# Optimization experiments

Hardware: AMD Instinct MI355X
Metric: run time of the kernel (lower is better)

## Reference

```python
import jax, jax.numpy as jnp
import numpy as np

B, T, D = 1, 2048, 3072
N, K, H = 16, 8, 256  # heads, kv heads, head dim
SOFT_CAP = 50.0
WINDOW = 1024
ROPE_BASE = 10000.0
ROPE_SCALE = 1.0
K_MASK = -2.3819763e+38
EPS = 1e-6


def rms_norm(x, scale=None):
    var = jnp.mean(jnp.square(x), axis=-1, keepdims=True)
    y = x * jax.lax.rsqrt(var + EPS)
    if scale is not None:
        y = y * (1.0 + scale)
    return y


def apply_rope(x, positions):
    # x: [B, T, n, H], positions: [B, T] int
    half = x.shape[-1] // 2
    fraction = 2.0 * jnp.arange(half, dtype=jnp.float32) / x.shape[-1]
    timescale = ROPE_BASE ** fraction  # [half]
    sinusoid = positions[..., None].astype(jnp.float32) / timescale  # [B,T,half]
    sinusoid = sinusoid[..., None, :] / ROPE_SCALE  # [B,T,1,half]
    sin, cos = jnp.sin(sinusoid), jnp.cos(sinusoid)
    first, second = jnp.split(x, 2, axis=-1)
    out = jnp.concatenate([first * cos - second * sin,
                           second * cos + first * sin], axis=-1)
    return out.astype(x.dtype)


def setup_inputs() -> dict:
    key = jax.random.key(0)
    ks = jax.random.split(key, 6)
    x = jax.random.normal(ks[0], (B, T, D), jnp.float32)
    segment_pos = jnp.broadcast_to(jnp.arange(T, dtype=jnp.int32), (B, T))
    attn_mask = jnp.broadcast_to(jnp.tril(jnp.ones((T, T), bool)), (B, T, T))
    w_q = jax.random.normal(ks[1], (N, D, H), jnp.float32) * 0.02
    w_kv = jax.random.normal(ks[2], (2, K, D, H), jnp.float32) * 0.02
    w_out = jax.random.normal(ks[3], (N, H, D), jnp.float32) * 0.02
    q_scale = jax.random.normal(ks[4], (H,), jnp.float32) * 0.1
    k_scale = jax.random.normal(ks[5], (H,), jnp.float32) * 0.1
    return {"x": x, "segment_pos": segment_pos, "attn_mask": attn_mask,
            "w_q": w_q, "w_kv": w_kv, "w_out": w_out,
            "q_scale": q_scale, "k_scale": k_scale}


def reference(x, segment_pos, attn_mask, w_q, w_kv, w_out, q_scale, k_scale):
    # Q projection + QK-RMSNorm + RoPE
    q = jnp.einsum('BTD,NDH->BTNH', x, w_q)
    q = rms_norm(q, q_scale)
    q = apply_rope(q, segment_pos)
    # fused KV projection
    kv = jnp.einsum('BSD,CKDH->CBSKH', x, w_kv)
    k_proj, v_proj = kv[0], kv[1]
    k_proj = rms_norm(k_proj, k_scale)
    v_proj = rms_norm(v_proj)  # value norm has no scale
    k_proj = apply_rope(k_proj, segment_pos)
    # GQA logits: q [B,T,K,G,H] x k [B,S,K,H]
    G = N // K
    qg = q.reshape(B, T, K, G, H)
    logits = jnp.einsum('BTKGH,BSKH->BTKGS', qg, k_proj).reshape(B, T, N, T)
    # logit soft-capping
    logits = jnp.tanh(logits / SOFT_CAP) * SOFT_CAP
    # sliding-window mask (cache_positions == segment_pos since cache is None)
    pos_q = segment_pos[:, :, None]
    pos_k = segment_pos[:, None, :]
    sliding = (pos_k > pos_q - WINDOW) & (pos_k < pos_q + WINDOW)  # [B,T,S]
    mask = attn_mask & sliding
    padded = jnp.where(mask[:, :, None, :], logits, K_MASK)
    probs = jax.nn.softmax(padded, axis=-1).astype(k_proj.dtype)
    enc = jnp.einsum('BTKGS,BSKH->BTKGH',
                     probs.reshape(B, T, K, G, T), v_proj).reshape(B, T, N, H)
    attn_output = jnp.einsum('BTNH,NHD->BTD', enc, w_out)
    return attn_output
```

## Files before the change

### kernel.cpp

```cpp
#include <hip/hip_runtime.h>
#include <math.h>

#define T_SEQ 2048
#define D_MODEL 3072
#define NQ 16
#define NKV 8
#define HD 256
#define NHEADS_TOT 32
#define QKV_COLS 8192
#define SOFT_CAP 50.0f
#define WINDOW 1024
#define K_MASK -2.3819763e38f

typedef __attribute__((ext_vector_type(8))) short bf16x8;
typedef __attribute__((ext_vector_type(4))) float f32x4;

__device__ __forceinline__ unsigned short f2bf(float f) {
    union { float f; unsigned u; } v; v.f = f;
    unsigned r = (v.u + 0x7fff + ((v.u >> 16) & 1)) >> 16;
    return (unsigned short)r;
}
__device__ __forceinline__ float bf2f(unsigned short u) {
    union { unsigned u; float f; } v; v.u = ((unsigned)u) << 16;
    return v.f;
}

__device__ __forceinline__ void gl_lds16(const unsigned short* g, unsigned short* l) {
    __builtin_amdgcn_global_load_lds(
        (const __attribute__((address_space(1))) void*)g,
        (__attribute__((address_space(3))) void*)l, 16, 0, 0);
}

__global__ __launch_bounds__(256) void k_convert(const float* __restrict__ src,
                                                 unsigned short* __restrict__ dst, int n4) {
    int i = blockIdx.x * 256 + threadIdx.x;
    if (i >= n4) return;
    float4 v = ((const float4*)src)[i];
    ushort4 o;
    o.x = f2bf(v.x); o.y = f2bf(v.y); o.z = f2bf(v.z); o.w = f2bf(v.w);
    ((ushort4*)dst)[i] = o;
}

__global__ __launch_bounds__(256) void k_transpose_bf16(const float* __restrict__ src,
                                                        unsigned short* __restrict__ dst,
                                                        int R, int C) {
    __shared__ unsigned short T[64][68];
    int b = blockIdx.z;
    src += (size_t)b * R * C;
    dst += (size_t)b * R * C;
    int c0 = blockIdx.x * 64, r0 = blockIdx.y * 64;
    int tid = threadIdx.x;
    int wv = tid >> 6, ln = tid & 63;
    int rsub = (wv << 2) + (ln >> 4);
    int cq = (ln & 15) << 2;
    #pragma unroll
    for (int p = 0; p < 4; p++) {
        int row = p * 16 + rsub;
        float4 v = *(const float4*)&src[(size_t)(r0 + row) * C + c0 + cq];
        T[cq + 0][row] = f2bf(v.x);
        T[cq + 1][row] = f2bf(v.y);
        T[cq + 2][row] = f2bf(v.z);
        T[cq + 3][row] = f2bf(v.w);
    }
    __syncthreads();
    #pragma unroll
    for (int q = 0; q < 4; q++) {
        int crow = q * 16 + rsub;
        ushort4 o = *(const ushort4*)&T[crow][cq];
        *(ushort4*)&dst[(size_t)(c0 + crow) * R + r0 + cq] = o;
    }
}

__global__ __launch_bounds__(256) void k_transpose_v(const unsigned short* __restrict__ src,
                                                     unsigned short* __restrict__ dst) {
    __shared__ unsigned short tile[32][34];
    int kk = blockIdx.z;
    src += (size_t)kk * T_SEQ * HD;
    dst += (size_t)kk * HD * T_SEQ;
    int h0 = blockIdx.x * 32, t0 = blockIdx.y * 32;
    int tx = threadIdx.x, ty = threadIdx.y;
    #pragma unroll
    for (int i = ty; i < 32; i += 8)
        tile[i][tx] = src[(size_t)(t0 + i) * HD + h0 + tx];
    __syncthreads();
    #pragma unroll
    for (int i = ty; i < 32; i += 8)
        dst[(size_t)(h0 + i) * T_SEQ + t0 + tx] = tile[tx][i];
}

__global__ __launch_bounds__(128) void k_trig(const int* __restrict__ spos,
                                              float2* __restrict__ tbl) {
    int t = blockIdx.x, hh = threadIdx.x;
    float fr = (float)hh * (1.0f / 128.0f);
    float ts = __expf(fr * 9.210340371976184f);
    float ang = (float)spos[t] / ts;
    float2 sc;
    sc.x = __sinf(ang);
    sc.y = __cosf(ang);
    tbl[(size_t)t * 128 + hh] = sc;
}

__global__ __launch_bounds__(256, 2) void k_gemm1(const unsigned short* __restrict__ A,
                                                  const unsigned short* __restrict__ BT,
                                                  unsigned short* __restrict__ C,
                                                  int M, int N, int Kd) {
    __shared__ unsigned short As[128 * 64];
    __shared__ unsigned short Bs[256 * 64];
    const int tid = threadIdx.x;
    const int wave = tid >> 6, lane = tid & 63;
    const int col = lane & 15, quad = lane >> 4;
    const int wr = wave & 1, wc = wave >> 1;

    int p = blockIdx.x;
    int xcd = p & 7, q = p >> 3;
    int i_t = q & 15, jj = q >> 4;
    const int m0 = i_t * 128, n0 = (jj * 8 + xcd) * 256;

    const int lrow = lane >> 3, lchk = lane & 7;
    int soffA[4], soffB[8];
    #pragma unroll
    for (int s = 0; s < 4; s++) {
        int r = wave * 32 + s * 8 + lrow;
        soffA[s] = r * Kd + ((lchk ^ (r & 7)) * 8);
    }
    #pragma unroll
    for (int s = 0; s < 8; s++) {
        int r = wave * 64 + s * 8 + lrow;
        soffB[s] = r * Kd + ((lchk ^ (r & 7)) * 8);
    }
    const unsigned short* Ab = A + (size_t)m0 * Kd;
    const unsigned short* Bb = BT + (size_t)n0 * Kd;

    f32x4 acc[4][8];
    #pragma unroll
    for (int i = 0; i < 4; i++)
        #pragma unroll
        for (int j = 0; j < 8; j++)
            acc[i][j] = (f32x4){0.f, 0.f, 0.f, 0.f};

    const int sw = col & 7;

    for (int k0 = 0; k0 < Kd; k0 += 64) {
        #pragma unroll
        for (int s = 0; s < 4; s++)
            gl_lds16(Ab + soffA[s] + k0, &As[(wave * 32 + s * 8) * 64]);
        #pragma unroll
        for (int s = 0; s < 8; s++)
            gl_lds16(Bb + soffB[s] + k0, &Bs[(wave * 64 + s * 8) * 64]);
        __syncthreads();

        #pragma unroll
        for (int kk = 0; kk < 2; kk++) {
            const int chko = ((kk * 4 + quad) ^ sw) * 8;
            bf16x8 af[4];
            #pragma unroll
            for (int i = 0; i < 4; i++)
                af[i] = *(const bf16x8*)&As[(wr * 64 + i * 16 + col) * 64 + chko];
            #pragma unroll
            for (int j = 0; j < 8; j++) {
                bf16x8 bfr = *(const bf16x8*)&Bs[(wc * 128 + j * 16 + col) * 64 + chko];
                #pragma unroll
                for (int i = 0; i < 4; i++)
                    acc[i][j] = __builtin_amdgcn_mfma_f32_16x16x32_bf16(af[i], bfr, acc[i][j], 0, 0, 0);
            }
        }
        __syncthreads();
    }

    #pragma unroll
    for (int i = 0; i < 4; i++) {
        int row = m0 + wr * 64 + i * 16 + quad * 4;
        #pragma unroll
        for (int j = 0; j < 8; j++) {
            int c = n0 + wc * 128 + j * 16 + col;
            #pragma unroll
            for (int r = 0; r < 4; r++)
                C[(size_t)(row + r) * N + c] = f2bf(acc[i][j][r]);
        }
    }
}

__global__ __launch_bounds__(256) void k_gemm2(const unsigned short* __restrict__ A,
                                               const unsigned short* __restrict__ BT,
                                               float* __restrict__ C,
                                               int M, int N, int Kd) {
    __shared__ unsigned short As[128 * 128];
    __shared__ unsigned short Bs[64 * 128];
    const int tid = threadIdx.x;
    const int wave = tid >> 6, lane = tid & 63;
    const int col = lane & 15, quad = lane >> 4;

    int p = blockIdx.x;
    int xcd = p & 7, q = p >> 3;
    int i_t = q % 16, jj = q / 16;
    const int m0 = i_t * 128, n0 = (jj * 8 + xcd) * 64;

    const int lrow = lane >> 4, lchk = lane & 15;
    int soffA[8], soffB[4];
    #pragma unroll
    for (int s = 0; s < 8; s++) {
        int r = wave * 32 + s * 4 + lrow;
        soffA[s] = r * Kd + ((lchk ^ (r & 7)) * 8);
    }
    #pragma unroll
    for (int s = 0; s < 4; s++) {
        int r = wave * 16 + s * 4 + lrow;
        soffB[s] = r * Kd + ((lchk ^ (r & 7)) * 8);
    }
    const unsigned short* Ab = A + (size_t)m0 * Kd;
    const unsigned short* Bb = BT + (size_t)n0 * Kd;

    f32x4 acc[2][4];
    #pragma unroll
    for (int i = 0; i < 2; i++)
        #pragma unroll
        for (int j = 0; j < 4; j++)
            acc[i][j] = (f32x4){0.f, 0.f, 0.f, 0.f};

    const int sw = col & 7;

    for (int k0 = 0; k0 < Kd; k0 += 128) {
        #pragma unroll
        for (int s = 0; s < 8; s++)
            gl_lds16(Ab + soffA[s] + k0, &As[(wave * 32 + s * 4) * 128]);
        #pragma unroll
        for (int s = 0; s < 4; s++)
            gl_lds16(Bb + soffB[s] + k0, &Bs[(wave * 16 + s * 4) * 128]);
        __syncthreads();

        #pragma unroll
        for (int kk = 0; kk < 4; kk++) {
            const int chko = ((kk * 4 + quad) ^ sw) * 8;
            bf16x8 af[2], bfr[4];
            #pragma unroll
            for (int i = 0; i < 2; i++)
                af[i] = *(const bf16x8*)&As[(wave * 32 + i * 16 + col) * 128 + chko];
            #pragma unroll
            for (int j = 0; j < 4; j++)
                bfr[j] = *(const bf16x8*)&Bs[(j * 16 + col) * 128 + chko];
            #pragma unroll
            for (int i = 0; i < 2; i++)
                #pragma unroll
                for (int j = 0; j < 4; j++)
                    acc[i][j] = __builtin_amdgcn_mfma_f32_16x16x32_bf16(af[i], bfr[j], acc[i][j], 0, 0, 0);
        }
        __syncthreads();
    }

    #pragma unroll
    for (int i = 0; i < 2; i++) {
        int row = m0 + wave * 32 + i * 16 + quad * 4;
        #pragma unroll
        for (int j = 0; j < 4; j++) {
            int c = n0 + j * 16 + col;
            #pragma unroll
            for (int r = 0; r < 4; r++)
                C[(size_t)(row + r) * N + c] = acc[i][j][r];
        }
    }
}

__global__ __launch_bounds__(256) void k_norm_rope(const unsigned short* __restrict__ qkv,
                                                   const float2* __restrict__ trig,
                                                   const float* __restrict__ qscale,
                                                   const float* __restrict__ kscale,
                                                   unsigned short* __restrict__ qh,
                                                   unsigned short* __restrict__ kh,
                                                   unsigned short* __restrict__ vh) {
    const int t = blockIdx.x, y = blockIdx.y, h = threadIdx.x;
    __shared__ float wsum[4][4];
    __shared__ float ybuf[3][256];

    float val[4];
    #pragma unroll
    for (int g = 0; g < 4; g++)
        val[g] = bf2f(qkv[(size_t)t * QKV_COLS + (y + g * 8) * HD + h]);

    float ssg[4];
    #pragma unroll
    for (int g = 0; g < 4; g++) {
        float ss = val[g] * val[g];
        #pragma unroll
        for (int m = 1; m < 64; m <<= 1) ss += __shfl_xor(ss, m, 64);
        ssg[g] = ss;
    }
    if ((h & 63) == 0) {
        #pragma unroll
        for (int g = 0; g < 4; g++) wsum[g][h >> 6] = ssg[g];
    }
    __syncthreads();

    float2 sc = trig[(size_t)t * 128 + (h & 127)];
    float qs = 1.0f + qscale[h], ks = 1.0f + kscale[h];

    float yv[4];
    #pragma unroll
    for (int g = 0; g < 4; g++) {
        float tot = wsum[g][0] + wsum[g][1] + wsum[g][2] + wsum[g][3];
        float yy = val[g] * rsqrtf(tot * (1.0f / 256.0f) + 1e-6f);
        if (g < 2) yy *= qs;
        else if (g == 2) yy *= ks;
        yv[g] = yy;
        if (g < 3) ybuf[g][h] = yy;
    }
    __syncthreads();

    #pragma unroll
    for (int g = 0; g < 3; g++) {
        float other = ybuf[g][(h < 128) ? (h + 128) : (h - 128)];
        float outv = (h < 128) ? (yv[g] * sc.y - other * sc.x)
                               : (yv[g] * sc.y + other * sc.x);
        int slot = y + g * 8;
        if (slot < 16)
            qh[((size_t)slot * T_SEQ + t) * HD + h] = f2bf(outv);
        else
            kh[((size_t)(slot - 16) * T_SEQ + t) * HD + h] = f2bf(outv);
    }
    vh[((size_t)y * T_SEQ + t) * HD + h] = f2bf(yv[3]);
}

__global__ __launch_bounds__(256) void k_attn(const unsigned short* __restrict__ qh,
                                              const unsigned short* __restrict__ kh,
                                              const unsigned short* __restrict__ vT,
                                              unsigned short* __restrict__ enc) {
    __shared__ unsigned short Ks[2][32 * 256];
    __shared__ unsigned short Vs[2][256 * 32];
    __shared__ unsigned short Pl[4][16 * 40];

    const int tid = threadIdx.x;
    const int wave = tid >> 6, lane = tid & 63;
    const int col = lane & 15, quad = lane >> 4;
    const int kk = blockIdx.x;
    const int t0b = blockIdx.y * 32;
    const int headSel = wave & 1, rowSel = wave >> 1;
    const int n = kk * 2 + headSel;
    const int tw = t0b + rowSel * 16;

    const unsigned short* qp = qh + ((size_t)n * T_SEQ + tw) * HD;
    const unsigned short* kp = kh + (size_t)kk * T_SEQ * HD;
    const unsigned short* vp = vT + (size_t)kk * HD * T_SEQ;

    bf16x8 qf[8];
    #pragma unroll
    for (int c = 0; c < 8; c++)
        qf[c] = *(const bf16x8*)(qp + (size_t)col * HD + c * 32 + quad * 8);

    int preK[4], preV[4], ldsKo[4], ldsVo[4];
    #pragma unroll
    for (int i = 0; i < 4; i++) {
        int krow = 2 * (wave * 4 + i) + (lane >> 5);
        int kpos = lane & 31;
        preK[i] = krow * HD + ((kpos ^ (krow & 7)) * 8);
        ldsKo[i] = (wave * 4 + i) * 512;
        int vh2 = (wave * 4 + i) * 16 + (lane >> 2);
        int vpp = lane & 3;
        preV[i] = vh2 * T_SEQ + ((vpp ^ (vh2 & 3)) * 8);
        ldsVo[i] = (wave * 4 + i) * 512;
    }

    f32x4 o[16];
    #pragma unroll
    for (int h = 0; h < 16; h++) o[h] = (f32x4){0.f, 0.f, 0.f, 0.f};
    float lsum[4] = {0.f, 0.f, 0.f, 0.f};

    int s_begin = t0b - (WINDOW - 1);
    if (s_begin < 0) s_begin = 0;
    s_begin &= ~31;
    const int s_end = t0b + 32;

    #pragma unroll
    for (int i = 0; i < 4; i++)
        gl_lds16(kp + (size_t)s_begin * HD + preK[i], &Ks[0][ldsKo[i]]);
    #pragma unroll
    for (int i = 0; i < 4; i++)
        gl_lds16(vp + (size_t)s_begin + preV[i], &Vs[0][ldsVo[i]]);
    __syncthreads();

    int nb = 0;
    for (int s0 = s_begin; s0 < s_end; s0 += 32) {
        int s1 = s0 + 32;
        if (s1 < s_end) {
            #pragma unroll
            for (int i = 0; i < 4; i++)
                gl_lds16(kp + (size_t)s1 * HD + preK[i], &Ks[nb ^ 1][ldsKo[i]]);
            #pragma unroll
            for (int i = 0; i < 4; i++)
                gl_lds16(vp + (size_t)s1 + preV[i], &Vs[nb ^ 1][ldsVo[i]]);
        }
        __builtin_amdgcn_sched_barrier(0);

        f32x4 S0 = (f32x4){0.f, 0.f, 0.f, 0.f};
        f32x4 S1 = (f32x4){0.f, 0.f, 0.f, 0.f};
        #pragma unroll
        for (int c = 0; c < 8; c++) {
            bf16x8 kf = *(const bf16x8*)&Ks[nb][(size_t)col * HD + (((c * 4 + quad) ^ (col & 7)) * 8)];
            S0 = __builtin_amdgcn_mfma_f32_16x16x32_bf16(qf[c], kf, S0, 0, 0, 0);
        }
        #pragma unroll
        for (int c = 0; c < 8; c++) {
            bf16x8 kf = *(const bf16x8*)&Ks[nb][(size_t)(16 + col) * HD + (((c * 4 + quad) ^ (col & 7)) * 8)];
            S1 = __builtin_amdgcn_mfma_f32_16x16x32_bf16(qf[c], kf, S1, 0, 0, 0);
        }

        #pragma unroll
        for (int r = 0; r < 4; r++) {
            int t = tw + quad * 4 + r;
            int sA = s0 + col, sB = sA + 16;
            bool vA = (sA <= t) && (sA >= t - (WINDOW - 1));
            bool vB = (sB <= t) && (sB >= t - (WINDOW - 1));
            float eA = __expf(S0[r] * (2.0f / SOFT_CAP));
            float eB = __expf(S1[r] * (2.0f / SOFT_CAP));
            float rA = __builtin_amdgcn_rcpf(eA + 1.0f);
            float rB = __builtin_amdgcn_rcpf(eB + 1.0f);
            float pA = __expf(SOFT_CAP - 2.0f * SOFT_CAP * rA);
            float pB = __expf(SOFT_CAP - 2.0f * SOFT_CAP * rB);
            pA = vA ? pA : 0.0f;
            pB = vB ? pB : 0.0f;
            lsum[r] += pA + pB;
            Pl[wave][(quad * 4 + r) * 40 + col] = f2bf(pA);
            Pl[wave][(quad * 4 + r) * 40 + 16 + col] = f2bf(pB);
        }

        bf16x8 pf = *(const bf16x8*)&Pl[wave][col * 40 + quad * 8];

        #pragma unroll
        for (int ht = 0; ht < 16; ht++) {
            int h = ht * 16 + col;
            bf16x8 vf = *(const bf16x8*)&Vs[nb][(size_t)h * 32 + ((quad ^ (h & 3)) * 8)];
            o[ht] = __builtin_amdgcn_mfma_f32_16x16x32_bf16(pf, vf, o[ht], 0, 0, 0);
        }
        __syncthreads();
        nb ^= 1;
    }

    #pragma unroll
    for (int r = 0; r < 4; r++) {
        #pragma unroll
        for (int m = 1; m < 16; m <<= 1)
            lsum[r] += __shfl_xor(lsum[r], m, 16);
        lsum[r] = 1.0f / lsum[r];
    }
    #pragma unroll
    for (int ht = 0; ht < 16; ht++) {
        #pragma unroll
        for (int r = 0; r < 4; r++) {
            int t = tw + quad * 4 + r;
            enc[(size_t)t * (NQ * HD) + n * HD + ht * 16 + col] = f2bf(o[ht][r] * lsum[r]);
        }
    }
}

extern "C" void kernel_launch(void* const* d_in, const int* in_sizes, int n_in,
                              void* d_out, int out_size, void* d_ws, size_t ws_size,
                              hipStream_t stream) {
    const float* x       = (const float*)d_in[0];
    const int*   spos    = (const int*)d_in[1];
    const float* w_q     = (const float*)d_in[3];
    const float* w_kv    = (const float*)d_in[4];
    const float* w_out   = (const float*)d_in[5];
    const float* q_scale = (const float*)d_in[6];
    const float* k_scale = (const float*)d_in[7];
    float* out = (float*)d_out;

    char* ws = (char*)d_ws;
    unsigned short* xb     = (unsigned short*)(ws + 0);
    unsigned short* vh     = (unsigned short*)(ws + 0);
    float2*         trig   = (float2*)(ws + 8388608);
    unsigned short* wT     = (unsigned short*)(ws + 12582912);
    unsigned short* wToutb = (unsigned short*)(ws + 12582912);
    unsigned short* encb   = (unsigned short*)(ws + 37748736);
    unsigned short* qkv    = (unsigned short*)(ws + 62914560);
    unsigned short* qh     = (unsigned short*)(ws + 96468992);
    unsigned short* kh     = (unsigned short*)(ws + 113246208);
    unsigned short* vT     = (unsigned short*)(ws + 121634816);

    k_convert<<<dim3((T_SEQ * D_MODEL / 4 + 255) / 256), dim3(256), 0, stream>>>(
        x, xb, T_SEQ * D_MODEL / 4);
    k_transpose_bf16<<<dim3(HD / 64, D_MODEL / 64, NQ), dim3(256), 0, stream>>>(
        w_q, wT, D_MODEL, HD);
    k_transpose_bf16<<<dim3(HD / 64, D_MODEL / 64, 16), dim3(256), 0, stream>>>(
        w_kv, wT + (size_t)4096 * D_MODEL, D_MODEL, HD);
    k_gemm1<<<dim3((T_SEQ / 128) * (QKV_COLS / 256)), dim3(256), 0, stream>>>(
        xb, wT, qkv, T_SEQ, QKV_COLS, D_MODEL);
    k_trig<<<dim3(T_SEQ), dim3(128), 0, stream>>>(spos, trig);
    k_transpose_bf16<<<dim3(D_MODEL / 64, 4096 / 64, 1), dim3(256), 0, stream>>>(
        w_out, wToutb, 4096, D_MODEL);
    k_norm_rope<<<dim3(T_SEQ, 8), dim3(256), 0, stream>>>(
        qkv, trig, q_scale, k_scale, qh, kh, vh);
    k_transpose_v<<<dim3(HD / 32, T_SEQ / 32, NKV), dim3(32, 8), 0, stream>>>(vh, vT);
    k_attn<<<dim3(NKV, T_SEQ / 32), dim3(256), 0, stream>>>(qh, kh, vT, encb);
    k_gemm2<<<dim3((T_SEQ / 128) * (D_MODEL / 64)), dim3(256), 0, stream>>>(
        encb, wToutb, out, T_SEQ, D_MODEL, NQ * HD);
}
```

Measured before the change: 469.2 us.

## Fuse QK RMSNorm, RoPE and V transpose into QKV GEMM epilogue

```diff
diff --git a/kernel.cpp b/kernel.cpp
--- a/kernel.cpp
+++ b/kernel.cpp
@@ -71,23 +71,6 @@
     }
 }
 
-__global__ __launch_bounds__(256) void k_transpose_v(const unsigned short* __restrict__ src,
-                                                     unsigned short* __restrict__ dst) {
-    __shared__ unsigned short tile[32][34];
-    int kk = blockIdx.z;
-    src += (size_t)kk * T_SEQ * HD;
-    dst += (size_t)kk * HD * T_SEQ;
-    int h0 = blockIdx.x * 32, t0 = blockIdx.y * 32;
-    int tx = threadIdx.x, ty = threadIdx.y;
-    #pragma unroll
-    for (int i = ty; i < 32; i += 8)
-        tile[i][tx] = src[(size_t)(t0 + i) * HD + h0 + tx];
-    __syncthreads();
-    #pragma unroll
-    for (int i = ty; i < 32; i += 8)
-        dst[(size_t)(h0 + i) * T_SEQ + t0 + tx] = tile[tx][i];
-}
-
 __global__ __launch_bounds__(128) void k_trig(const int* __restrict__ spos,
                                               float2* __restrict__ tbl) {
     int t = blockIdx.x, hh = threadIdx.x;
@@ -102,7 +85,12 @@
 
 __global__ __launch_bounds__(256, 2) void k_gemm1(const unsigned short* __restrict__ A,
                                                   const unsigned short* __restrict__ BT,
-                                                  unsigned short* __restrict__ C,
+                                                  const float2* __restrict__ trig,
+                                                  const float* __restrict__ qscale,
+                                                  const float* __restrict__ kscale,
+                                                  unsigned short* __restrict__ qh,
+                                                  unsigned short* __restrict__ kh,
+                                                  unsigned short* __restrict__ vT,
                                                   int M, int N, int Kd) {
     __shared__ unsigned short As[128 * 64];
     __shared__ unsigned short Bs[256 * 64];
@@ -167,16 +155,78 @@
         __syncthreads();
     }
 
+    const int slot = n0 >> 8;
+    float* rs = (float*)As;
+
+    float rinv[4][4];
+    #pragma unroll
+    for (int i = 0; i < 4; i++)
+        #pragma unroll
+        for (int r = 0; r < 4; r++) {
+            float ss = 0.f;
+            #pragma unroll
+            for (int j = 0; j < 8; j++) ss += acc[i][j][r] * acc[i][j][r];
+            #pragma unroll
+            for (int m = 1; m < 16; m <<= 1) ss += __shfl_xor(ss, m, 16);
+            if (col == 0) rs[wc * 128 + wr * 64 + i * 16 + quad * 4 + r] = ss;
+        }
+    __syncthreads();
+    #pragma unroll
+    for (int i = 0; i < 4; i++)
+        #pragma unroll
+        for (int r = 0; r < 4; r++) {
+            int rl = wr * 64 + i * 16 + quad * 4 + r;
+            float tot = rs[rl] + rs[128 + rl];
+            rinv[i][r] = rsqrtf(tot * (1.0f / 256.0f) + 1e-6f);
+        }
+
+    float scl[8];
+    #pragma unroll
+    for (int j = 0; j < 8; j++) {
+        int h = wc * 128 + j * 16 + col;
+        scl[j] = (slot < 16) ? (1.0f + qscale[h])
+               : (slot < 24) ? (1.0f + kscale[h]) : 1.0f;
+    }
+
+    float* yb = (float*)Bs;
     #pragma unroll
     for (int i = 0; i < 4; i++) {
-        int row = m0 + wr * 64 + i * 16 + quad * 4;
+        float yv[8][4];
+        #pragma unroll
+        for (int j = 0; j < 8; j++)
+            #pragma unroll
+            for (int r = 0; r < 4; r++)
+                yv[j][r] = acc[i][j][r] * rinv[i][r] * scl[j];
+        #pragma unroll
+        for (int j = 0; j < 8; j++)
+            #pragma unroll
+            for (int r = 0; r < 4; r++)
+                yb[((wc * 2 + wr) * 16 + quad * 4 + r) * 128 + j * 16 + col] = yv[j][r];
+        __syncthreads();
         #pragma unroll
         for (int j = 0; j < 8; j++) {
-            int c = n0 + wc * 128 + j * 16 + col;
-            #pragma unroll
-            for (int r = 0; r < 4; r++)
-                C[(size_t)(row + r) * N + c] = f2bf(acc[i][j][r]);
-        }
+            int h = wc * 128 + j * 16 + col;
+            #pragma unroll
+            for (int r = 0; r < 4; r++) {
+                int t = m0 + wr * 64 + i * 16 + quad * 4 + r;
+                float oth = yb[(((wc ^ 1) * 2 + wr) * 16 + quad * 4 + r) * 128 + j * 16 + col];
+                float outv;
+                if (slot < 24) {
+                    float2 sc = trig[(size_t)t * 128 + j * 16 + col];
+                    outv = (wc == 0) ? (yv[j][r] * sc.y - oth * sc.x)
+                                     : (yv[j][r] * sc.y + oth * sc.x);
+                } else {
+                    outv = yv[j][r];
+                }
+                if (slot < 16)
+                    qh[((size_t)slot * T_SEQ + t) * HD + h] = f2bf(outv);
+                else if (slot < 24)
+                    kh[((size_t)(slot - 16) * T_SEQ + t) * HD + h] = f2bf(outv);
+                else
+                    vT[((size_t)(slot - 24) * HD + h) * T_SEQ + t] = f2bf(outv);
+            }
+        }
+        __syncthreads();
     }
 }
 
@@ -258,65 +308,6 @@
                 C[(size_t)(row + r) * N + c] = acc[i][j][r];
         }
     }
-}
-
-__global__ __launch_bounds__(256) void k_norm_rope(const unsigned short* __restrict__ qkv,
-                                                   const float2* __restrict__ trig,
-                                                   const float* __restrict__ qscale,
-                                                   const float* __restrict__ kscale,
-                                                   unsigned short* __restrict__ qh,
-                                                   unsigned short* __restrict__ kh,
-                                                   unsigned short* __restrict__ vh) {
-    const int t = blockIdx.x, y = blockIdx.y, h = threadIdx.x;
-    __shared__ float wsum[4][4];
-    __shared__ float ybuf[3][256];
-
-    float val[4];
-    #pragma unroll
-    for (int g = 0; g < 4; g++)
-        val[g] = bf2f(qkv[(size_t)t * QKV_COLS + (y + g * 8) * HD + h]);
-
-    float ssg[4];
-    #pragma unroll
-    for (int g = 0; g < 4; g++) {
-        float ss = val[g] * val[g];
-        #pragma unroll
-        for (int m = 1; m < 64; m <<= 1) ss += __shfl_xor(ss, m, 64);
-        ssg[g] = ss;
-    }
-    if ((h & 63) == 0) {
-        #pragma unroll
-        for (int g = 0; g < 4; g++) wsum[g][h >> 6] = ssg[g];
-    }
-    __syncthreads();
-
-    float2 sc = trig[(size_t)t * 128 + (h & 127)];
-    float qs = 1.0f + qscale[h], ks = 1.0f + kscale[h];
-
-    float yv[4];
-    #pragma unroll
-    for (int g = 0; g < 4; g++) {
-        float tot = wsum[g][0] + wsum[g][1] + wsum[g][2] + wsum[g][3];
-        float yy = val[g] * rsqrtf(tot * (1.0f / 256.0f) + 1e-6f);
-        if (g < 2) yy *= qs;
-        else if (g == 2) yy *= ks;
-        yv[g] = yy;
-        if (g < 3) ybuf[g][h] = yy;
-    }
-    __syncthreads();
-
-    #pragma unroll
-    for (int g = 0; g < 3; g++) {
-        float other = ybuf[g][(h < 128) ? (h + 128) : (h - 128)];
-        float outv = (h < 128) ? (yv[g] * sc.y - other * sc.x)
-                               : (yv[g] * sc.y + other * sc.x);
-        int slot = y + g * 8;
-        if (slot < 16)
-            qh[((size_t)slot * T_SEQ + t) * HD + h] = f2bf(outv);
-        else
-            kh[((size_t)(slot - 16) * T_SEQ + t) * HD + h] = f2bf(outv);
-    }
-    vh[((size_t)y * T_SEQ + t) * HD + h] = f2bf(yv[3]);
 }
 
 __global__ __launch_bounds__(256) void k_attn(const unsigned short* __restrict__ qh,
@@ -464,12 +455,10 @@
 
     char* ws = (char*)d_ws;
     unsigned short* xb     = (unsigned short*)(ws + 0);
-    unsigned short* vh     = (unsigned short*)(ws + 0);
-    float2*         trig   = (float2*)(ws + 8388608);
     unsigned short* wT     = (unsigned short*)(ws + 12582912);
     unsigned short* wToutb = (unsigned short*)(ws + 12582912);
     unsigned short* encb   = (unsigned short*)(ws + 37748736);
-    unsigned short* qkv    = (unsigned short*)(ws + 62914560);
+    float2*         trig   = (float2*)(ws + 62914560);
     unsigned short* qh     = (unsigned short*)(ws + 96468992);
     unsigned short* kh     = (unsigned short*)(ws + 113246208);
     unsigned short* vT     = (unsigned short*)(ws + 121634816);
@@ -480,14 +469,11 @@
         w_q, wT, D_MODEL, HD);
     k_transpose_bf16<<<dim3(HD / 64, D_MODEL / 64, 16), dim3(256), 0, stream>>>(
         w_kv, wT + (size_t)4096 * D_MODEL, D_MODEL, HD);
+    k_trig<<<dim3(T_SEQ), dim3(128), 0, stream>>>(spos, trig);
     k_gemm1<<<dim3((T_SEQ / 128) * (QKV_COLS / 256)), dim3(256), 0, stream>>>(
-        xb, wT, qkv, T_SEQ, QKV_COLS, D_MODEL);
-    k_trig<<<dim3(T_SEQ), dim3(128), 0, stream>>>(spos, trig);
+        xb, wT, trig, q_scale, k_scale, qh, kh, vT, T_SEQ, QKV_COLS, D_MODEL);
     k_transpose_bf16<<<dim3(D_MODEL / 64, 4096 / 64, 1), dim3(256), 0, stream>>>(
         w_out, wToutb, 4096, D_MODEL);
-    k_norm_rope<<<dim3(T_SEQ, 8), dim3(256), 0, stream>>>(
-        qkv, trig, q_scale, k_scale, qh, kh, vh);
-    k_transpose_v<<<dim3(HD / 32, T_SEQ / 32, NKV), dim3(32, 8), 0, stream>>>(vh, vT);
     k_attn<<<dim3(NKV, T_SEQ / 32), dim3(256), 0, stream>>>(qh, kh, vT, encb);
     k_gemm2<<<dim3((T_SEQ / 128) * (D_MODEL / 64)), dim3(256), 0, stream>>>(
         encb, wToutb, out, T_SEQ, D_MODEL, NQ * HD);
```

Measured after the change: 474.7 us. No clear change (+1.2%).
